# Performance work log

Measured on AMD Instinct MI355X. Metric: run time of the kernel, lower is better.

The kernel has to match this reference:

```python
import jax, jax.numpy as jnp
import numpy as np

N = 12  # mmse_block_size
REAL_SIZE = N * (N + 1) // 2  # 78: diag + strict lower
IMAG_SIZE = N * (N - 1) // 2  # 66: strict lower only
ROWS, COLS = jnp.tril_indices(N)        # row-major (i, j<=i) matches torch loop order
ROWS_S, COLS_S = jnp.tril_indices(N, -1)  # strict lower, row-major, matches imag loop
DIAG_MASK = jnp.eye(N, dtype=bool)


def _mlp(x, W1, b1, W2, b2, W3, b3):
    h = jax.nn.relu(x @ W1 + b1)
    h = jax.nn.relu(h @ W2 + b2)
    return h @ W3 + b3


def _cholesky_outer(flat):
    # flat: [B, REAL_SIZE + IMAG_SIZE] -> [B, N, N] complex, L @ L^H
    B = flat.shape[0]
    L_real = jnp.zeros((B, N, N), flat.dtype).at[:, ROWS, COLS].set(flat[:, :REAL_SIZE])
    L_real = jnp.where(DIAG_MASK, jax.nn.softplus(L_real), L_real)
    L_imag = jnp.zeros((B, N, N), flat.dtype).at[:, ROWS_S, COLS_S].set(
        flat[:, REAL_SIZE:REAL_SIZE + IMAG_SIZE])
    L = L_real + 1j * L_imag
    return jnp.einsum('bij,bkj->bik', L, jnp.conj(L))


def setup_inputs() -> dict:
    key = jax.random.key(0)
    ks = jax.random.split(key, 13)
    L, H, OUT = 4096, 64, REAL_SIZE + IMAG_SIZE
    sc = lambda k, shp, fan: (jax.random.normal(k, shp, jnp.float32) / np.sqrt(fan))
    return {
        'channel_stats': jax.random.normal(ks[0], (8192, L), jnp.float32),
        'WC1': sc(ks[1], (L, H), L), 'bC1': jnp.zeros((H,), jnp.float32),
        'WC2': sc(ks[2], (H, H), H), 'bC2': jnp.zeros((H,), jnp.float32),
        'WC3': sc(ks[3], (H, OUT), H), 'bC3': jnp.zeros((OUT,), jnp.float32),
        'WR1': sc(ks[4], (L, H), L), 'bR1': jnp.zeros((H,), jnp.float32),
        'WR2': sc(ks[5], (H, H), H), 'bR2': jnp.zeros((H,), jnp.float32),
        'WR3': sc(ks[6], (H, OUT), H), 'bR3': jnp.zeros((OUT,), jnp.float32),
    }


def reference(channel_stats, WC1, bC1, WC2, bC2, WC3, bC3,
              WR1, bR1, WR2, bR2, WR3, bR3):
    C_flat = _mlp(channel_stats, WC1, bC1, WC2, bC2, WC3, bC3)
    R_flat = _mlp(channel_stats, WR1, bR1, WR2, bR2, WR3, bR3)
    C = _cholesky_outer(C_flat)
    R = _cholesky_outer(R_flat)
    return C, R
```

## Files before the change

kernel.cpp:

```cpp
#include <hip/hip_runtime.h>
#include <stdint.h>

#define M_ROWS 8192
#define K_DIM  4096
#define OUTD   144
#define PLANE  1179648
#define NT2    8

typedef __attribute__((ext_vector_type(4))) float  float4v;
typedef __attribute__((ext_vector_type(8))) short  short8v;

static __device__ __forceinline__ unsigned short f2bf(float f) {
    unsigned int u = __builtin_bit_cast(unsigned int, f);
    u += 0x7FFFu + ((u >> 16) & 1u);
    return (unsigned short)(u >> 16);
}

__global__ __launch_bounds__(256) void wt_kernel(
    const float* __restrict__ WC1, const float* __restrict__ WR1,
    unsigned short* __restrict__ Wt) {
    __shared__ float tile[64][65];
    const float* src = (blockIdx.y == 0) ? WC1 : WR1;
    const int k0 = blockIdx.x * 64;
    const int t = threadIdx.x;
    const int j = t & 63, qq = t >> 6;
#pragma unroll
    for (int p = 0; p < 16; ++p) {
        int i = p * 4 + qq;
        tile[i][j] = src[(size_t)(k0 + i) * 64 + j];
    }
    __syncthreads();
    const int tt  = blockIdx.x >> 1;
    const int ksb = (blockIdx.x & 1) * 2;
#pragma unroll
    for (int p = 0; p < 16; ++p) {
        int c = p * 256 + t;
        int e = c & 7, m = (c >> 3) & 15, q = (c >> 7) & 3;
        int ks_l = (c >> 9) & 1, w_l = (c >> 10) & 3;
        int kp = ks_l * 32 + q * 8 + e;
        int np = w_l * 16 + m;
        int wg = blockIdx.y * 4 + w_l;
        size_t dst = ((size_t)(wg * 32 + tt) * 4 + (ksb + ks_l)) * 512
                   + q * 128 + m * 8 + e;
        Wt[dst] = f2bf(tile[kp][np]);
    }
}


#define ISSUE_B(TB_, B0_, B1_, B2_, B3_)                         \
    do { const unsigned short* bp_ = bpw + (size_t)(TB_) * 2048; \
         B0_ = *(const short8v*)(bp_ + 0 * 512);                 \
         B1_ = *(const short8v*)(bp_ + 1 * 512);                 \
         B2_ = *(const short8v*)(bp_ + 2 * 512);                 \
         B3_ = *(const short8v*)(bp_ + 3 * 512); } while (0)

#define ISSUE_A(T_, XA_, XB_, XC_, XD_)                          \
    do { const float* ap_ = xpw + (size_t)(T_) * 512;            \
         XA_ = *(const float4*)(ap_);                            \
         XB_ = *(const float4*)(ap_ + 4);                        \
         XC_ = *(const float4*)(ap_ + 256);                      \
         XD_ = *(const float4*)(ap_ + 260); } while (0)

#define STORE_A(BUF_, XA_, XB_, XC_, XD_)                              \
    do { short8v s1_, s2_;                                             \
         s1_[0] = (short)f2bf((XA_).x); s1_[1] = (short)f2bf((XA_).y); \
         s1_[2] = (short)f2bf((XA_).z); s1_[3] = (short)f2bf((XA_).w); \
         s1_[4] = (short)f2bf((XB_).x); s1_[5] = (short)f2bf((XB_).y); \
         s1_[6] = (short)f2bf((XB_).z); s1_[7] = (short)f2bf((XB_).w); \
         s2_[0] = (short)f2bf((XC_).x); s2_[1] = (short)f2bf((XC_).y); \
         s2_[2] = (short)f2bf((XC_).z); s2_[3] = (short)f2bf((XC_).w); \
         s2_[4] = (short)f2bf((XD_).x); s2_[5] = (short)f2bf((XD_).y); \
         s2_[6] = (short)f2bf((XD_).z); s2_[7] = (short)f2bf((XD_).w); \
         *(short8v*)(Asm_ + (BUF_) * 8192 + (w * 64 + lane) * 8) = s1_; \
         *(short8v*)(Asm_ + (BUF_) * 8192 + 4096 + (w * 64 + lane) * 8) = s2_; } while (0)

#define MFR(BUF_, SUB_, B0_, B1_, B2_, B3_)                                    \
    do { const unsigned short* ab_ = Asm_ + (BUF_) * 8192 + (SUB_) * 2048 + lane * 8; \
         short8v a0_ = *(const short8v*)(ab_ + 0 * 512);                       \
         short8v a1_ = *(const short8v*)(ab_ + 1 * 512);                       \
         short8v a2_ = *(const short8v*)(ab_ + 2 * 512);                       \
         short8v a3_ = *(const short8v*)(ab_ + 3 * 512);                       \
         acc = __builtin_amdgcn_mfma_f32_16x16x32_bf16(a0_, B0_, acc, 0, 0, 0);\
         acc = __builtin_amdgcn_mfma_f32_16x16x32_bf16(a1_, B1_, acc, 0, 0, 0);\
         acc = __builtin_amdgcn_mfma_f32_16x16x32_bf16(a2_, B2_, acc, 0, 0, 0);\
         acc = __builtin_amdgcn_mfma_f32_16x16x32_bf16(a3_, B3_, acc, 0, 0, 0);\
    } while (0)

__global__ __launch_bounds__(512, 4) void fused_kernel(
    const float* __restrict__ X, const unsigned short* __restrict__ Wt,
    const float* __restrict__ bC1, const float* __restrict__ bR1,
    const float* __restrict__ WC2, const float* __restrict__ bC2,
    const float* __restrict__ WR2, const float* __restrict__ bR2,
    const float* __restrict__ WC3, const float* __restrict__ bC3,
    const float* __restrict__ WR3, const float* __restrict__ bR3,
    unsigned short* __restrict__ OUT) {
    __shared__ __align__(16) char smem[41216];
    unsigned short* Asm_ = (unsigned short*)smem;
    float* hs  = (float*)smem;
    float* W2s = hs + 16 * 132;
    float* fl  = W2s;

    const int tid  = threadIdx.x;
    const int lane = tid & 63;
    const int w    = tid >> 6;
    const int r0   = blockIdx.x * 16;
    const int m    = lane & 15, q = lane >> 4;

    float4v acc = {0.f, 0.f, 0.f, 0.f};

    const unsigned short* bpw = Wt + (size_t)w * 32 * 2048 + lane * 8;
    const float* xpw = X + (size_t)(r0 + m) * K_DIM + w * 32 + q * 8;

    short8v b00, b01, b02, b03, b10, b11, b12, b13;
    short8v b20, b21, b22, b23, b30, b31, b32, b33;
    float4 xa0, xa1, xa2, xa3;

    ISSUE_A(0, xa0, xa1, xa2, xa3);

#pragma unroll 1
    for (int t = 0; t < NT2; ++t) {
        const int buf = t & 1;
        STORE_A(buf, xa0, xa1, xa2, xa3);
        if (t + 1 < NT2) ISSUE_A(t + 1, xa0, xa1, xa2, xa3);
        asm volatile("s_waitcnt lgkmcnt(0)" ::: "memory");
        __builtin_amdgcn_s_barrier();
        __builtin_amdgcn_sched_barrier(0);
        ISSUE_B(t * 4 + 0, b00, b01, b02, b03);
        ISSUE_B(t * 4 + 1, b10, b11, b12, b13);
        ISSUE_B(t * 4 + 2, b20, b21, b22, b23);
        ISSUE_B(t * 4 + 3, b30, b31, b32, b33);
        MFR(buf, 0, b00, b01, b02, b03);
        MFR(buf, 1, b10, b11, b12, b13);
        MFR(buf, 2, b20, b21, b22, b23);
        MFR(buf, 3, b30, b31, b32, b33);
    }
    __syncthreads();

    {
        const int c = w * 16 + m;
        const float bv = (c < 64) ? bC1[c] : bR1[c - 64];
#pragma unroll
        for (int i = 0; i < 4; ++i) {
            int r = q * 4 + i;
            float v = acc[i] + bv; v = v > 0.f ? v : 0.f;
            hs[r * 132 + c] = v;
        }
    }
#pragma unroll
    for (int p = 0; p < 4; ++p) {
        int fi = p * 512 + tid;
        int k = fi >> 5, c4 = fi & 31;
        int c = c4 * 4;
        const float* wsrc = (c < 64) ? (WC2 + (size_t)k * 64 + c)
                                     : (WR2 + (size_t)k * 64 + (c - 64));
        *(float4*)&W2s[k * 128 + c] = *(const float4*)wsrc;
    }
    __syncthreads();

    const int rg = tid >> 5;
    const int cg = tid & 31;
    const int koff2 = (cg < 16) ? 0 : 64;
    float acc2[4];
    {
        int c = cg * 4;
        const float* bsrc = (c < 64) ? (bC2 + c) : (bR2 + (c - 64));
#pragma unroll
        for (int j = 0; j < 4; ++j) acc2[j] = bsrc[j];
    }
    for (int k = 0; k < 64; ++k) {
        float4 wv = *(const float4*)&W2s[k * 128 + cg * 4];
        float a = hs[rg * 132 + koff2 + k];
        acc2[0] += a * wv.x; acc2[1] += a * wv.y;
        acc2[2] += a * wv.z; acc2[3] += a * wv.w;
    }
    float4 h2v;
    h2v.x = acc2[0] > 0.f ? acc2[0] : 0.f;
    h2v.y = acc2[1] > 0.f ? acc2[1] : 0.f;
    h2v.z = acc2[2] > 0.f ? acc2[2] : 0.f;
    h2v.w = acc2[3] > 0.f ? acc2[3] : 0.f;
    __syncthreads();
    *(float4*)&hs[rg * 132 + cg * 4] = h2v;
    __syncthreads();

#pragma unroll 1
    for (int pass = 0; pass < 3; ++pass) {
        int c = pass * 128 + cg * 4;
        if (c < 288) {
            const int brn = (c >= 144);
            const int cl = c - (brn ? 144 : 0);
            const float* W3 = brn ? WR3 : WC3;
            const float* b3 = brn ? bR3 : bC3;
            const int ko = brn ? 64 : 0;
            float a3[4];
#pragma unroll
            for (int j = 0; j < 4; ++j) a3[j] = b3[cl + j];
            for (int k = 0; k < 64; ++k) {
                float4 wv = *(const float4*)(W3 + (size_t)k * OUTD + cl);
                float a = hs[rg * 132 + ko + k];
                a3[0] += a * wv.x; a3[1] += a * wv.y;
                a3[2] += a * wv.z; a3[3] += a * wv.w;
            }
            float4 v; v.x = a3[0]; v.y = a3[1]; v.z = a3[2]; v.w = a3[3];
            *(float4*)&fl[rg * 288 + c] = v;
        }
    }
    __syncthreads();

    if (tid < 384) {
        int r = tid / 24, rem = tid % 24;
        int brn = rem / 12, ii = rem % 12;
        float* f = &fl[r * 288 + brn * 144];
        int d = ii * (ii + 1) / 2 + ii;
        float xv = f[d];
        f[d] = (xv > 20.f) ? xv : log1pf(expf(xv));
    }
    __syncthreads();

    unsigned int* O32 = (unsigned int*)OUT;
    for (int task = tid; task < 16 * 2 * 78; task += 512) {
        int r = task / 156, rem = task % 156;
        int brn = rem / 78, p = rem % 78;
        int i = 0;
        while (p >= (i + 1) * (i + 2) / 2) ++i;
        int j = p - i * (i + 1) / 2;
        const float* f = &fl[r * 288 + brn * 144];
        const float* g = f + 78;
        const int ti = i * (i + 1) / 2, tj = j * (j + 1) / 2;
        const int si = i * (i - 1) / 2, sj = j * (j - 1) / 2;
        float re = 0.f, im = 0.f;
        for (int k = 0; k <= j; ++k) {
            float ar_ = f[ti + k];
            float ai  = (k == i) ? 0.f : g[si + k];
            float br_ = f[tj + k];
            float bi  = (k == j) ? 0.f : g[sj + k];
            re += ar_ * br_ + ai * bi;
            im += ai * br_ - ar_ * bi;
        }
        unsigned int reb = (unsigned int)f2bf(re);
        unsigned int imb = (unsigned int)f2bf(im);
        unsigned int imn = (unsigned int)f2bf(-im);
        size_t base = brn ? (size_t)PLANE : 0;
        size_t q1 = (size_t)(r0 + r) * 144 + (size_t)(i * 12 + j);
        O32[base + q1] = imb | (reb << 16);
        if (i != j) {
            size_t q2 = (size_t)(r0 + r) * 144 + (size_t)(j * 12 + i);
            O32[base + q2] = imn | (reb << 16);
        }
    }
}

extern "C" void kernel_launch(void* const* d_in, const int* in_sizes, int n_in,
                              void* d_out, int out_size, void* d_ws, size_t ws_size,
                              hipStream_t stream) {
    const float* X   = (const float*)d_in[0];
    const float* WC1 = (const float*)d_in[1];
    const float* bC1 = (const float*)d_in[2];
    const float* WC2 = (const float*)d_in[3];
    const float* bC2 = (const float*)d_in[4];
    const float* WC3 = (const float*)d_in[5];
    const float* bC3 = (const float*)d_in[6];
    const float* WR1 = (const float*)d_in[7];
    const float* bR1 = (const float*)d_in[8];
    const float* WR2 = (const float*)d_in[9];
    const float* bR2 = (const float*)d_in[10];
    const float* WR3 = (const float*)d_in[11];
    const float* bR3 = (const float*)d_in[12];

    unsigned short* Wt = (unsigned short*)d_ws;
    unsigned short* OUT = (unsigned short*)d_out;

    wt_kernel<<<dim3(64, 2), 256, 0, stream>>>(WC1, WR1, Wt);
    fused_kernel<<<M_ROWS / 16, 512, 0, stream>>>(
        X, Wt, bC1, bR1, WC2, bC2, WR2, bR2, WC3, bC3, WR3, bR3, OUT);
}
```

Before: 262.1 us.

## Split fused MLP kernel into GEMM1 kernel and separate tail kernel

Splits the single fused kernel into two launches. The first runs the large bf16 MFMA GEMM and writes the ReLU hidden activations into a spare region of the output buffer. The second reloads them and runs layers 2-3 and the Cholesky outer product. The aim is to keep the GEMM kernel's LDS footprint and register pressure small, so more blocks stay resident during the memory-bound phase and the tail's LDS needs stop limiting it. The cost is an extra launch and a round trip of the hidden activations through global memory, and the scratch in the output plane must be overwritten correctly afterward.

```diff
diff --git a/kernel.cpp b/kernel.cpp
--- a/kernel.cpp
+++ b/kernel.cpp
@@ -86,19 +86,11 @@
          acc = __builtin_amdgcn_mfma_f32_16x16x32_bf16(a3_, B3_, acc, 0, 0, 0);\
     } while (0)
 
-__global__ __launch_bounds__(512, 4) void fused_kernel(
+__global__ __launch_bounds__(512, 4) void gemm1_kernel(
     const float* __restrict__ X, const unsigned short* __restrict__ Wt,
     const float* __restrict__ bC1, const float* __restrict__ bR1,
-    const float* __restrict__ WC2, const float* __restrict__ bC2,
-    const float* __restrict__ WR2, const float* __restrict__ bR2,
-    const float* __restrict__ WC3, const float* __restrict__ bC3,
-    const float* __restrict__ WR3, const float* __restrict__ bR3,
-    unsigned short* __restrict__ OUT) {
-    __shared__ __align__(16) char smem[41216];
-    unsigned short* Asm_ = (unsigned short*)smem;
-    float* hs  = (float*)smem;
-    float* W2s = hs + 16 * 132;
-    float* fl  = W2s;
+    unsigned int* __restrict__ O32) {
+    __shared__ __align__(16) unsigned short Asm_[2 * 8192];
 
     const int tid  = threadIdx.x;
     const int lane = tid & 63;
@@ -134,17 +126,39 @@
         MFR(buf, 2, b20, b21, b22, b23);
         MFR(buf, 3, b30, b31, b32, b33);
     }
-    __syncthreads();
 
     {
         const int c = w * 16 + m;
         const float bv = (c < 64) ? bC1[c] : bR1[c - 64];
 #pragma unroll
         for (int i = 0; i < 4; ++i) {
-            int r = q * 4 + i;
+            int r = r0 + q * 4 + i;
             float v = acc[i] + bv; v = v > 0.f ? v : 0.f;
-            hs[r * 132 + c] = v;
-        }
+            O32[(size_t)PLANE + (size_t)144 * r + c] =
+                __builtin_bit_cast(unsigned int, v);
+        }
+    }
+}
+
+__global__ __launch_bounds__(512) void tail_kernel(
+    const float* __restrict__ WC2, const float* __restrict__ bC2,
+    const float* __restrict__ WR2, const float* __restrict__ bR2,
+    const float* __restrict__ WC3, const float* __restrict__ bC3,
+    const float* __restrict__ WR3, const float* __restrict__ bR3,
+    unsigned int* __restrict__ O32) {
+    __shared__ __align__(16) char smem[41216];
+    float* hs  = (float*)smem;
+    float* W2s = hs + 16 * 132;
+    float* fl  = W2s;
+
+    const int tid = threadIdx.x;
+    const int r0  = blockIdx.x * 16;
+
+    {
+        int row = tid >> 5, qd = tid & 31;
+        const float* h1p =
+            (const float*)(O32 + (size_t)PLANE + (size_t)144 * (r0 + row));
+        *(float4*)&hs[row * 132 + qd * 4] = *(const float4*)(h1p + qd * 4);
     }
 #pragma unroll
     for (int p = 0; p < 4; ++p) {
@@ -216,7 +230,6 @@
     }
     __syncthreads();
 
-    unsigned int* O32 = (unsigned int*)OUT;
     for (int task = tid; task < 16 * 2 * 78; task += 512) {
         int r = task / 156, rem = task % 156;
         int brn = rem / 78, p = rem % 78;
@@ -266,10 +279,11 @@
     const float* WR3 = (const float*)d_in[11];
     const float* bR3 = (const float*)d_in[12];
 
-    unsigned short* Wt = (unsigned short*)d_ws;
-    unsigned short* OUT = (unsigned short*)d_out;
+    unsigned short* Wt  = (unsigned short*)d_ws;
+    unsigned int*   O32 = (unsigned int*)d_out;
 
     wt_kernel<<<dim3(64, 2), 256, 0, stream>>>(WC1, WR1, Wt);
-    fused_kernel<<<M_ROWS / 16, 512, 0, stream>>>(
-        X, Wt, bC1, bR1, WC2, bC2, WR2, bR2, WC3, bC3, WR3, bR3, OUT);
-}
+    gemm1_kernel<<<M_ROWS / 16, 512, 0, stream>>>(X, Wt, bC1, bR1, O32);
+    tail_kernel<<<M_ROWS / 16, 512, 0, stream>>>(
+        WC2, bC2, WR2, bR2, WC3, bC3, WR3, bR3, O32);
+}
```

After: 270.9 us. 1.03x slower.
